# Performance work log

Hardware: AMD Instinct MI355X
Metric: run time of the kernel (lower is better)

The kernel has to match this reference:

```python
import jax, jax.numpy as jnp
import numpy as np

ROPE_THETA = 10000.0

def apply_rope(x, positions):
    # x: [b, h, s, d], positions: [s]
    d = x.shape[-1]
    inv_freq = ROPE_THETA ** (-jnp.arange(0, d, 2, dtype=jnp.float32) / d)  # [d/2]
    ang = positions.astype(jnp.float32)[:, None] * inv_freq[None, :]        # [s, d/2]
    cos = jnp.cos(ang)
    sin = jnp.sin(ang)
    x1 = x[..., 0::2]
    x2 = x[..., 1::2]
    r1 = x1 * cos - x2 * sin
    r2 = x1 * sin + x2 * cos
    # interleave back to [..., d]
    return jnp.stack([r1, r2], axis=-1).reshape(x.shape)

def setup_inputs() -> dict:
    key = jax.random.key(0)
    k1, k2, k3 = jax.random.split(key, 3)
    b, s, d_model = 4, 2048, 1024
    x = jax.random.normal(k1, (b, s, d_model), dtype=jnp.float32)
    wqkv = jax.random.normal(k2, (3 * d_model, d_model), dtype=jnp.float32) * (d_model ** -0.5)
    wo = jax.random.normal(k3, (d_model, d_model), dtype=jnp.float32) * (d_model ** -0.5)
    token_positions = jnp.arange(s, dtype=jnp.int64 if jax.config.jax_enable_x64 else jnp.int32)
    return {"x": x, "wqkv": wqkv, "wo": wo, "token_positions": token_positions}

def reference(x, wqkv, wo, token_positions):
    b, s, d_model = x.shape
    num_heads = 16
    d_head = d_model // num_heads
    # fused QKV projection (Linear: y = x @ W.T)
    qkv = jnp.einsum('bse,fe->bsf', x, wqkv)  # [b, s, 3*d_model]
    q, k, v = jnp.split(qkv, 3, axis=-1)
    def to_heads(t):
        return t.reshape(b, s, num_heads, d_head).transpose(0, 2, 1, 3)  # [b, h, s, d]
    q, k, v = to_heads(q), to_heads(k), to_heads(v)
    q = apply_rope(q, token_positions)
    k = apply_rope(k, token_positions)
    scores = jnp.einsum('bhqd,bhkd->bhqk', q, k) / jnp.sqrt(jnp.asarray(d_head, dtype=x.dtype))
    causal = jnp.tril(jnp.ones((s, s), dtype=bool))  # [s, s]
    scores = jnp.where(causal, scores, -jnp.inf)
    weights = jax.nn.softmax(scores, axis=-1)
    y = jnp.einsum('bhqk,bhkd->bhqd', weights, v)
    y = y.transpose(0, 2, 1, 3).reshape(b, s, d_model)
    return jnp.einsum('bse,fe->bsf', y, wo)
```

## Files before the change

### kernel.cpp

```cpp
#include <hip/hip_runtime.h>
#include <stdint.h>


typedef __attribute__((ext_vector_type(8))) short bf16x8;
typedef __attribute__((ext_vector_type(4))) float f32x4;
typedef __attribute__((ext_vector_type(8))) unsigned short u16x8;
typedef __attribute__((ext_vector_type(4))) unsigned short u16x4;

#define NB 4
#define NS 2048
#define NH 16
#define DH 64
#define DM 1024
#define BH (NB*NH)

static __device__ __forceinline__ unsigned short f2bf(float f){
  unsigned u = __builtin_bit_cast(unsigned, f);
  u += 0x7fffu + ((u >> 16) & 1u);
  return (unsigned short)(u >> 16);
}
static __device__ __forceinline__ float bf2f(unsigned short h){
  unsigned u = ((unsigned)h) << 16;
  return __builtin_bit_cast(float, u);
}
static __device__ __forceinline__ unsigned cvt_pk_bf16(float lo, float hi){
  unsigned r;
  asm("v_cvt_pk_bf16_f32 %0, %1, %2" : "=v"(r) : "v"(lo), "v"(hi));
  return r;
}
static __device__ __forceinline__ f32x4 mfma16(bf16x8 a, bf16x8 b, f32x4 c){
  return __builtin_amdgcn_mfma_f32_16x16x32_bf16(a, b, c, 0, 0, 0);
}
static __device__ __forceinline__ void gld_lds16(const void* g, void* l){
  __builtin_amdgcn_global_load_lds((const __attribute__((address_space(1))) unsigned int*)g,
                                   (__attribute__((address_space(3))) unsigned int*)l,
                                   16, 0, 0);
}

__global__ __launch_bounds__(256) void cvt_all(const float* __restrict__ x,
                                               const float* __restrict__ wqkv,
                                               const float* __restrict__ wo,
                                               unsigned short* __restrict__ xb,
                                               unsigned short* __restrict__ wqkvb,
                                               unsigned short* __restrict__ wob){
  int stride = gridDim.x * blockDim.x;
  for (int i = blockIdx.x * blockDim.x + threadIdx.x; i < 3145728; i += stride){
    const float* src; unsigned short* dst; int j;
    if (i < 2097152){ src = x; dst = xb; j = i; }
    else if (i < 2883584){ src = wqkv; dst = wqkvb; j = i - 2097152; }
    else { src = wo; dst = wob; j = i - 2883584; }
    f32x4 v = *(const f32x4*)(src + (size_t)j * 4);
    u16x4 o;
    o[0] = f2bf(v[0]); o[1] = f2bf(v[1]); o[2] = f2bf(v[2]); o[3] = f2bf(v[3]);
    *(u16x4*)(dst + (size_t)j * 4) = o;
  }
}

__global__ void rope_table(const int* __restrict__ pos,
                           float* __restrict__ ct, float* __restrict__ st){
  int t = blockIdx.x * 256 + threadIdx.x;
  int s = t >> 5, i = t & 31;
  float p = (float)pos[s];
  float freq = exp2f(-(float)(2 * i) * (13.287712379549449f / 64.f));
  float a = p * freq;
  ct[t] = cosf(a);
  st[t] = sinf(a);
}

__global__ __launch_bounds__(256) void rope_qk(unsigned short* __restrict__ buf,
                                               const float* __restrict__ ct,
                                               const float* __restrict__ st){
  size_t t  = (size_t)blockIdx.x * 256 + threadIdx.x;
  size_t e0 = t * 8;
  int dh0 = (int)(e0 & 63);
  int s   = (int)((e0 >> 6) & (NS - 1));
  u16x8 v = *(const u16x8*)(buf + e0);
  f32x4 c  = *(const f32x4*)(ct + s * 32 + (dh0 >> 1));
  f32x4 sn = *(const f32x4*)(st + s * 32 + (dh0 >> 1));
  u16x8 o;
#pragma unroll
  for (int i = 0; i < 4; i++){
    float x1 = bf2f(v[2*i]), x2 = bf2f(v[2*i+1]);
    o[2*i]   = f2bf(x1 * c[i] - x2 * sn[i]);
    o[2*i+1] = f2bf(x1 * sn[i] + x2 * c[i]);
  }
  *(u16x8*)(buf + e0) = o;
}

template<int BM, int BN, int MF, int NFR, int EPI, int RING>
__global__ __launch_bounds__((BM/(MF*16))*(BN/(NFR*16))*64, 2)
void gemm_ring(const unsigned short* __restrict__ A,
               const unsigned short* __restrict__ Bm,
               void* __restrict__ out0, void* __restrict__ out1,
               void* __restrict__ out2, int M, int N, int K){
  constexpr int WM = BM / (MF * 16);
  constexpr int WN = BN / (NFR * 16);
  constexpr int T  = WM * WN * 64;
  constexpr int LA = BM * 4 / T;
  constexpr int LB = BN * 4 / T;
  constexpr int L  = LA + LB;
  __shared__ __attribute__((aligned(16))) unsigned short As[RING][BM * 32];
  __shared__ __attribute__((aligned(16))) unsigned short Bs[RING][BN * 32];
  int tid = threadIdx.x;
  int w = tid >> 6, l = tid & 63;
  int lr = l & 15, lk = l >> 4;
  int m0 = blockIdx.y * BM, n0 = blockIdx.x * BN;
  int wr = (w / WN) * (MF * 16), wc = (w % WN) * (NFR * 16);

  const int nt = K >> 5;

  auto stage = [&](int t, int buf){
    int k0 = t * 32;
#pragma unroll
    for (int i = 0; i < LA; i++){
      int f = i * T + tid;
      int row = f >> 2, c = f & 3;
      int gc = (c ^ ((row >> 1) & 3)) * 8;
      gld_lds16(A + (size_t)(m0 + row) * K + k0 + gc, &As[buf][(i * T + w * 64) * 8]);
    }
#pragma unroll
    for (int i = 0; i < LB; i++){
      int f = i * T + tid;
      int row = f >> 2, c = f & 3;
      int gc = (c ^ ((row >> 1) & 3)) * 8;
      gld_lds16(Bm + (size_t)(n0 + row) * K + k0 + gc, &Bs[buf][(i * T + w * 64) * 8]);
    }
  };

  f32x4 zero = {0.f, 0.f, 0.f, 0.f};
  f32x4 acc[MF][NFR];
#pragma unroll
  for (int a = 0; a < MF; a++)
#pragma unroll
    for (int b = 0; b < NFR; b++) acc[a][b] = zero;

#pragma unroll
  for (int p = 0; p < RING - 1; p++) stage(p, p);
  asm volatile("s_waitcnt vmcnt(%0)" :: "i"((RING - 2) * L) : "memory");
  __builtin_amdgcn_sched_barrier(0);
  __builtin_amdgcn_s_barrier();
  __builtin_amdgcn_sched_barrier(0);

  int buf = 0;
  for (int t = 0; t < nt; ++t){
    bf16x8 af[MF], bfr[NFR];
#pragma unroll
    for (int mf = 0; mf < MF; mf++){
      int row = wr + mf * 16 + lr;
      af[mf] = *(const bf16x8*)&As[buf][row * 32 + ((lk ^ ((row >> 1) & 3)) * 8)];
    }
#pragma unroll
    for (int nf = 0; nf < NFR; nf++){
      int row = wc + nf * 16 + lr;
      bfr[nf] = *(const bf16x8*)&Bs[buf][row * 32 + ((lk ^ ((row >> 1) & 3)) * 8)];
    }
    if (t + RING - 1 < nt){
      int sb = buf - 1; if (sb < 0) sb = RING - 1;
      stage(t + RING - 1, sb);
    }
    __builtin_amdgcn_s_setprio(1);
#pragma unroll
    for (int mf = 0; mf < MF; mf++)
#pragma unroll
      for (int nf = 0; nf < NFR; nf++)
        acc[mf][nf] = mfma16(af[mf], bfr[nf], acc[mf][nf]);
    __builtin_amdgcn_s_setprio(0);
    if (RING >= 4){
      if (t + 3 < nt)      { asm volatile("s_waitcnt vmcnt(%0)" :: "i"(2 * L) : "memory"); }
      else if (t + 2 < nt) { asm volatile("s_waitcnt vmcnt(%0)" :: "i"(L) : "memory"); }
      else if (t + 1 < nt) { asm volatile("s_waitcnt vmcnt(0)" ::: "memory"); }
    } else {
      if (t + 2 < nt)      { asm volatile("s_waitcnt vmcnt(%0)" :: "i"(L) : "memory"); }
      else if (t + 1 < nt) { asm volatile("s_waitcnt vmcnt(0)" ::: "memory"); }
    }
    __builtin_amdgcn_sched_barrier(0);
    __builtin_amdgcn_s_barrier();
    __builtin_amdgcn_sched_barrier(0);
    buf = buf + 1; if (buf == RING) buf = 0;
  }

  if (EPI == 0){
    unsigned short* q  = (unsigned short*)out0;
    unsigned short* k  = (unsigned short*)out1;
    unsigned short* vt = (unsigned short*)out2;
#pragma unroll
    for (int mf = 0; mf < MF; mf++)
#pragma unroll
      for (int nf = 0; nf < NFR; nf++)
#pragma unroll
        for (int j = 0; j < 4; j++){
          int m = m0 + wr + mf * 16 + lk * 4 + j;
          int n = n0 + wc + nf * 16 + lr;
          int part = n >> 10, c = n & 1023;
          int h = c >> 6, dh = c & 63;
          int b = m >> 11, s = m & (NS - 1);
          unsigned short val = f2bf(acc[mf][nf][j]);
          if (part == 2){
            vt[((size_t)((b * NH + h) * DH + dh)) * NS + s] = val;
          } else {
            size_t off = ((size_t)(b * NH + h) * NS + s) * DH + dh;
            ((part == 0) ? q : k)[off] = val;
          }
        }
  } else {
    float* C = (float*)out0;
#pragma unroll
    for (int mf = 0; mf < MF; mf++)
#pragma unroll
      for (int nf = 0; nf < NFR; nf++)
#pragma unroll
        for (int j = 0; j < 4; j++){
          int m = m0 + wr + mf * 16 + lk * 4 + j;
          int n = n0 + wc + nf * 16 + lr;
          C[(size_t)m * N + n] = acc[mf][nf][j];
        }
  }
}

__global__ __launch_bounds__(256, 3) void fa_kernel(const unsigned short* __restrict__ qb_,
                                                    const unsigned short* __restrict__ kbuf,
                                                    const unsigned short* __restrict__ vtb,
                                                    unsigned short* __restrict__ yb){
  __shared__ __attribute__((aligned(16))) unsigned short Kl[2][4096];
  __shared__ __attribute__((aligned(16))) unsigned short Vl[2][4096];
  __shared__ __attribute__((aligned(16))) unsigned short Pl[4][32 * 76];
  int tid = threadIdx.x;
  int w = tid >> 6, l = tid & 63;
  int lr = l & 15, lk = l >> 4;
  int qb = 15 - blockIdx.y;
  int bh = blockIdx.x;
  int b = bh >> 4, h = bh & 15;
  int qr0 = qb * 128 + w * 32;
  const unsigned short* Q  = qb_  + (size_t)bh * NS * DH;
  const unsigned short* Kp = kbuf + (size_t)bh * NS * DH;
  const unsigned short* VT = vtb  + (size_t)bh * DH * NS;
  unsigned short* Pw = &Pl[w][0];

  int r8  = l >> 3;
  int swc = ((l & 7) ^ (r8 & 7)) * 8;

  auto stage = [&](int buf, int t){
    int kbase = t * 64;
    if (w < 2){
#pragma unroll
      for (int ii = 0; ii < 4; ii++){
        int i = w * 4 + ii;
        gld_lds16(Kp + (size_t)(kbase + i * 8 + r8) * DH + swc, &Kl[buf][i * 512]);
      }
    } else {
#pragma unroll
      for (int ii = 0; ii < 4; ii++){
        int i = (w - 2) * 4 + ii;
        gld_lds16(VT + (size_t)(i * 8 + r8) * NS + kbase + swc, &Vl[buf][i * 512]);
      }
    }
  };

  bf16x8 qf[2][2];
#pragma unroll
  for (int mf = 0; mf < 2; mf++)
#pragma unroll
    for (int ks = 0; ks < 2; ks++)
      qf[mf][ks] = *(const bf16x8*)(Q + (size_t)(qr0 + mf * 16 + lr) * DH + ks * 32 + lk * 8);

  f32x4 zero = {0.f, 0.f, 0.f, 0.f};
  f32x4 O[2][4];
  float lsum[2];
#pragma unroll
  for (int mf = 0; mf < 2; mf++){
#pragma unroll
    for (int nf = 0; nf < 4; nf++) O[mf][nf] = zero;
    lsum[mf] = 0.f;
  }

  const float SC = 0.18033688011112042f;
  const int ntile = 2 * qb + 2;

  stage(0, 0);
  __syncthreads();

  int cur = 0;
  for (int t = 0; t < ntile; ++t){
    int kbase = t * 64;
    if (t + 1 < ntile) stage(cur ^ 1, t + 1);

    if (kbase <= qr0 + 31){
      bf16x8 kf[4][2];
#pragma unroll
      for (int nf = 0; nf < 4; nf++){
        int row = nf * 16 + lr;
        int ro = row * 64, sw = (row & 7) << 3;
#pragma unroll
        for (int ks = 0; ks < 2; ks++)
          kf[nf][ks] = *(const bf16x8*)&Kl[cur][ro + ((ks * 32 + lk * 8) ^ sw)];
      }
      bf16x8 vf[2][4];
#pragma unroll
      for (int nfd = 0; nfd < 4; nfd++){
        int row = nfd * 16 + lr;
        int ro = row * 64, sw = (row & 7) << 3;
#pragma unroll
        for (int ks = 0; ks < 2; ks++)
          vf[ks][nfd] = *(const bf16x8*)&Vl[cur][ro + ((ks * 32 + lk * 8) ^ sw)];
      }

      f32x4 sa[2][4];
#pragma unroll
      for (int mf = 0; mf < 2; mf++)
#pragma unroll
        for (int nf = 0; nf < 4; nf++) sa[mf][nf] = zero;
#pragma unroll
      for (int nf = 0; nf < 4; nf++)
#pragma unroll
        for (int mf = 0; mf < 2; mf++){
          sa[mf][nf] = mfma16(kf[nf][0], qf[mf][0], sa[mf][nf]);
          sa[mf][nf] = mfma16(kf[nf][1], qf[mf][1], sa[mf][nf]);
        }

      bool domask = (kbase + 63 > qr0);

#pragma unroll
      for (int mf = 0; mf < 2; mf++){
        int qg = qr0 + mf * 16 + lr;
        float ls = 0.f;
#pragma unroll
        for (int nf = 0; nf < 4; nf++){
          float p4[4];
#pragma unroll
          for (int j = 0; j < 4; j++){
            float xx = __builtin_fmaf(sa[mf][nf][j], SC, -8.0f);
            if (domask){
              int kg = kbase + nf * 16 + lk * 4 + j;
              if (kg > qg) xx = -__builtin_inff();
            }
            float p = exp2f(xx);
            ls += p;
            p4[j] = p;
          }
          unsigned d0 = cvt_pk_bf16(p4[0], p4[1]);
          unsigned d1 = cvt_pk_bf16(p4[2], p4[3]);
          int base = (mf * 16 + lr) * 76 + nf * 16 + lk * 4;
          *(unsigned*)&Pw[base]     = d0;
          *(unsigned*)&Pw[base + 2] = d1;
        }
        lsum[mf] += ls;
      }

      bf16x8 pf[2][2];
#pragma unroll
      for (int mf = 0; mf < 2; mf++)
#pragma unroll
        for (int ks = 0; ks < 2; ks++)
          pf[mf][ks] = *(const bf16x8*)&Pw[(mf * 16 + lr) * 76 + ks * 32 + lk * 8];
#pragma unroll
      for (int ks = 0; ks < 2; ks++)
#pragma unroll
        for (int nfd = 0; nfd < 4; nfd++)
#pragma unroll
          for (int mf = 0; mf < 2; mf++)
            O[mf][nfd] = mfma16(pf[mf][ks], vf[ks][nfd], O[mf][nfd]);
    }

    __syncthreads();
    cur ^= 1;
  }

#pragma unroll
  for (int mf = 0; mf < 2; mf++){
    lsum[mf] += __shfl_xor(lsum[mf], 16);
    lsum[mf] += __shfl_xor(lsum[mf], 32);
  }
#pragma unroll
  for (int mf = 0; mf < 2; mf++)
#pragma unroll
    for (int j = 0; j < 4; j++){
      float s = __shfl(lsum[mf], lk * 4 + j);
      float inv = 1.0f / s;
      int srow = qr0 + mf * 16 + lk * 4 + j;
      unsigned short* yp = yb + ((size_t)(b * NS + srow)) * DM + h * DH;
#pragma unroll
      for (int nfd = 0; nfd < 4; nfd++)
        yp[nfd * 16 + lr] = f2bf(O[mf][nfd][j] * inv);
    }
}

extern "C" void kernel_launch(void* const* d_in, const int* in_sizes, int n_in,
                              void* d_out, int out_size, void* d_ws, size_t ws_size,
                              hipStream_t stream){
  const float* x    = (const float*)d_in[0];
  const float* wqkv = (const float*)d_in[1];
  const float* wo   = (const float*)d_in[2];
  const int*   pos  = (const int*)d_in[3];
  float* out = (float*)d_out;

  char* ws = (char*)d_ws;
  size_t off = 0;
  auto alloc = [&](size_t bytes) -> void* {
    void* p = ws + off;
    off += (bytes + 255) & ~(size_t)255;
    return p;
  };
  const size_t NE = (size_t)BH * NS * DH;
  unsigned short* xb    = (unsigned short*)alloc((size_t)8192 * 1024 * 2);
  unsigned short* wqkvb = (unsigned short*)alloc((size_t)3072 * 1024 * 2);
  unsigned short* wob   = (unsigned short*)alloc((size_t)1024 * 1024 * 2);
  unsigned short* q  = (unsigned short*)alloc(NE * 2);
  unsigned short* k  = (unsigned short*)alloc(NE * 2);
  unsigned short* vt = (unsigned short*)alloc(NE * 2);
  unsigned short* y  = (unsigned short*)alloc(NE * 2);
  float* ct = (float*)alloc((size_t)NS * 32 * 4);
  float* st = (float*)alloc((size_t)NS * 32 * 4);

  cvt_all<<<3072, 256, 0, stream>>>(x, wqkv, wo, xb, wqkvb, wob);
  rope_table<<<256, 256, 0, stream>>>(pos, ct, st);
  gemm_ring<128, 256, 8, 4, 0, 3><<<dim3(12, 64), 256, 0, stream>>>(
      xb, wqkvb, q, k, vt, 8192, 3072, 1024);
  rope_qk<<<4096, 256, 0, stream>>>(q, ct, st);
  rope_qk<<<4096, 256, 0, stream>>>(k, ct, st);
  fa_kernel<<<dim3(64, 16), 256, 0, stream>>>(q, k, vt, y);
  gemm_ring<128, 128, 4, 4, 1, 4><<<dim3(8, 64), 256, 0, stream>>>(
      y, wob, out, nullptr, nullptr, 8192, 1024, 1024);
}
```

Before: 228.4 us.

## Load V fragments directly from global in attention and retune GEMM tiles

The attention kernel no longer stages V^T tiles through LDS. Each wave reads its V fragments straight from global memory, and all four waves now share the K staging. This cuts LDS use, shrinks the P scratch padding, and raises the occupancy hint to 4. The QKV GEMM moves from 128x256 to 128x128 tiles with more blocks and an occupancy hint of 3. The trade-off is that V loads now come from global or L2 inside the inner loop with their latency exposed, and the P padding change may cause LDS bank conflicts.

```diff
diff --git a/kernel.cpp b/kernel.cpp
--- a/kernel.cpp
+++ b/kernel.cpp
@@ -87,8 +87,8 @@
   *(u16x8*)(buf + e0) = o;
 }
 
-template<int BM, int BN, int MF, int NFR, int EPI, int RING>
-__global__ __launch_bounds__((BM/(MF*16))*(BN/(NFR*16))*64, 2)
+template<int BM, int BN, int MF, int NFR, int EPI, int RING, int OCC>
+__global__ __launch_bounds__((BM/(MF*16))*(BN/(NFR*16))*64, OCC)
 void gemm_ring(const unsigned short* __restrict__ A,
                const unsigned short* __restrict__ Bm,
                void* __restrict__ out0, void* __restrict__ out1,
@@ -217,13 +217,12 @@
   }
 }
 
-__global__ __launch_bounds__(256, 3) void fa_kernel(const unsigned short* __restrict__ qb_,
+__global__ __launch_bounds__(256, 4) void fa_kernel(const unsigned short* __restrict__ qb_,
                                                     const unsigned short* __restrict__ kbuf,
                                                     const unsigned short* __restrict__ vtb,
                                                     unsigned short* __restrict__ yb){
   __shared__ __attribute__((aligned(16))) unsigned short Kl[2][4096];
-  __shared__ __attribute__((aligned(16))) unsigned short Vl[2][4096];
-  __shared__ __attribute__((aligned(16))) unsigned short Pl[4][32 * 76];
+  __shared__ __attribute__((aligned(16))) unsigned short Pl[4][32 * 72];
   int tid = threadIdx.x;
   int w = tid >> 6, l = tid & 63;
   int lr = l & 15, lk = l >> 4;
@@ -241,18 +240,10 @@
 
   auto stage = [&](int buf, int t){
     int kbase = t * 64;
-    if (w < 2){
-#pragma unroll
-      for (int ii = 0; ii < 4; ii++){
-        int i = w * 4 + ii;
-        gld_lds16(Kp + (size_t)(kbase + i * 8 + r8) * DH + swc, &Kl[buf][i * 512]);
-      }
-    } else {
-#pragma unroll
-      for (int ii = 0; ii < 4; ii++){
-        int i = (w - 2) * 4 + ii;
-        gld_lds16(VT + (size_t)(i * 8 + r8) * NS + kbase + swc, &Vl[buf][i * 512]);
-      }
+#pragma unroll
+    for (int ii = 0; ii < 2; ii++){
+      int i = w * 2 + ii;
+      gld_lds16(Kp + (size_t)(kbase + i * 8 + r8) * DH + swc, &Kl[buf][i * 512]);
     }
   };
 
@@ -285,6 +276,13 @@
     if (t + 1 < ntile) stage(cur ^ 1, t + 1);
 
     if (kbase <= qr0 + 31){
+      bf16x8 vf[2][4];
+#pragma unroll
+      for (int ks = 0; ks < 2; ks++)
+#pragma unroll
+        for (int nfd = 0; nfd < 4; nfd++)
+          vf[ks][nfd] = *(const bf16x8*)(VT + (size_t)(nfd * 16 + lr) * NS + kbase + ks * 32 + lk * 8);
+
       bf16x8 kf[4][2];
 #pragma unroll
       for (int nf = 0; nf < 4; nf++){
@@ -293,15 +291,6 @@
 #pragma unroll
         for (int ks = 0; ks < 2; ks++)
           kf[nf][ks] = *(const bf16x8*)&Kl[cur][ro + ((ks * 32 + lk * 8) ^ sw)];
-      }
-      bf16x8 vf[2][4];
-#pragma unroll
-      for (int nfd = 0; nfd < 4; nfd++){
-        int row = nfd * 16 + lr;
-        int ro = row * 64, sw = (row & 7) << 3;
-#pragma unroll
-        for (int ks = 0; ks < 2; ks++)
-          vf[ks][nfd] = *(const bf16x8*)&Vl[cur][ro + ((ks * 32 + lk * 8) ^ sw)];
       }
 
       f32x4 sa[2][4];
@@ -337,11 +326,10 @@
             ls += p;
             p4[j] = p;
           }
-          unsigned d0 = cvt_pk_bf16(p4[0], p4[1]);
-          unsigned d1 = cvt_pk_bf16(p4[2], p4[3]);
-          int base = (mf * 16 + lr) * 76 + nf * 16 + lk * 4;
-          *(unsigned*)&Pw[base]     = d0;
-          *(unsigned*)&Pw[base + 2] = d1;
+          uint2 dd;
+          dd.x = cvt_pk_bf16(p4[0], p4[1]);
+          dd.y = cvt_pk_bf16(p4[2], p4[3]);
+          *(uint2*)&Pw[(mf * 16 + lr) * 72 + nf * 16 + lk * 4] = dd;
         }
         lsum[mf] += ls;
       }
@@ -351,7 +339,7 @@
       for (int mf = 0; mf < 2; mf++)
 #pragma unroll
         for (int ks = 0; ks < 2; ks++)
-          pf[mf][ks] = *(const bf16x8*)&Pw[(mf * 16 + lr) * 76 + ks * 32 + lk * 8];
+          pf[mf][ks] = *(const bf16x8*)&Pw[(mf * 16 + lr) * 72 + ks * 32 + lk * 8];
 #pragma unroll
       for (int ks = 0; ks < 2; ks++)
 #pragma unroll
@@ -413,11 +401,11 @@
 
   cvt_all<<<3072, 256, 0, stream>>>(x, wqkv, wo, xb, wqkvb, wob);
   rope_table<<<256, 256, 0, stream>>>(pos, ct, st);
-  gemm_ring<128, 256, 8, 4, 0, 3><<<dim3(12, 64), 256, 0, stream>>>(
+  gemm_ring<128, 128, 4, 4, 0, 3, 3><<<dim3(24, 64), 256, 0, stream>>>(
       xb, wqkvb, q, k, vt, 8192, 3072, 1024);
   rope_qk<<<4096, 256, 0, stream>>>(q, ct, st);
   rope_qk<<<4096, 256, 0, stream>>>(k, ct, st);
   fa_kernel<<<dim3(64, 16), 256, 0, stream>>>(q, k, vt, y);
-  gemm_ring<128, 128, 4, 4, 1, 4><<<dim3(8, 64), 256, 0, stream>>>(
+  gemm_ring<128, 128, 4, 4, 1, 4, 2><<<dim3(8, 64), 256, 0, stream>>>(
       y, wob, out, nullptr, nullptr, 8192, 1024, 1024);
 }
```

After: 252.7 us. +10.7%, slower.

## Fuse Q RoPE into attention Q load and retile QKV GEMM

Applied to the files above, without the earlier changes.

Removes the separate RoPE pass over Q by applying the rotation with the cos/sin tables while loading Q fragments inside the attention kernel, which saves a full read-modify-write of the Q buffer. It also changes the QKV projection GEMM from 128x256 to 128x128 tiles with a doubled grid and an occupancy hint of 3, via a new OCC template parameter on launch bounds. The extra rotation math in the attention prologue is small. The smaller GEMM tiles give more blocks and occupancy but less data reuse per tile.

```diff
diff --git a/kernel.cpp b/kernel.cpp
--- a/kernel.cpp
+++ b/kernel.cpp
@@ -6,6 +6,7 @@
 typedef __attribute__((ext_vector_type(4))) float f32x4;
 typedef __attribute__((ext_vector_type(8))) unsigned short u16x8;
 typedef __attribute__((ext_vector_type(4))) unsigned short u16x4;
+typedef __attribute__((ext_vector_type(4))) unsigned int u32x4;
 
 #define NB 4
 #define NS 2048
@@ -87,8 +88,8 @@
   *(u16x8*)(buf + e0) = o;
 }
 
-template<int BM, int BN, int MF, int NFR, int EPI, int RING>
-__global__ __launch_bounds__((BM/(MF*16))*(BN/(NFR*16))*64, 2)
+template<int BM, int BN, int MF, int NFR, int EPI, int RING, int OCC>
+__global__ __launch_bounds__((BM/(MF*16))*(BN/(NFR*16))*64, OCC)
 void gemm_ring(const unsigned short* __restrict__ A,
                const unsigned short* __restrict__ Bm,
                void* __restrict__ out0, void* __restrict__ out1,
@@ -220,7 +221,9 @@
 __global__ __launch_bounds__(256, 3) void fa_kernel(const unsigned short* __restrict__ qb_,
                                                     const unsigned short* __restrict__ kbuf,
                                                     const unsigned short* __restrict__ vtb,
-                                                    unsigned short* __restrict__ yb){
+                                                    unsigned short* __restrict__ yb,
+                                                    const float* __restrict__ ct_,
+                                                    const float* __restrict__ st_){
   __shared__ __attribute__((aligned(16))) unsigned short Kl[2][4096];
   __shared__ __attribute__((aligned(16))) unsigned short Vl[2][4096];
   __shared__ __attribute__((aligned(16))) unsigned short Pl[4][32 * 76];
@@ -258,10 +261,25 @@
 
   bf16x8 qf[2][2];
 #pragma unroll
-  for (int mf = 0; mf < 2; mf++)
-#pragma unroll
-    for (int ks = 0; ks < 2; ks++)
-      qf[mf][ks] = *(const bf16x8*)(Q + (size_t)(qr0 + mf * 16 + lr) * DH + ks * 32 + lk * 8);
+  for (int mf = 0; mf < 2; mf++){
+    int srow = qr0 + mf * 16 + lr;
+    const unsigned short* qrow = Q + (size_t)srow * DH;
+    const float* ctr = ct_ + srow * 32;
+    const float* str = st_ + srow * 32;
+#pragma unroll
+    for (int ks = 0; ks < 2; ks++){
+      u16x8 raw = *(const u16x8*)(qrow + ks * 32 + lk * 8);
+      f32x4 cc = *(const f32x4*)(ctr + ks * 16 + lk * 4);
+      f32x4 ss = *(const f32x4*)(str + ks * 16 + lk * 4);
+      u32x4 wds;
+#pragma unroll
+      for (int p = 0; p < 4; p++){
+        float x1 = bf2f(raw[2*p]), x2 = bf2f(raw[2*p+1]);
+        wds[p] = cvt_pk_bf16(x1 * cc[p] - x2 * ss[p], x1 * ss[p] + x2 * cc[p]);
+      }
+      qf[mf][ks] = __builtin_bit_cast(bf16x8, wds);
+    }
+  }
 
   f32x4 zero = {0.f, 0.f, 0.f, 0.f};
   f32x4 O[2][4];
@@ -413,11 +431,10 @@
 
   cvt_all<<<3072, 256, 0, stream>>>(x, wqkv, wo, xb, wqkvb, wob);
   rope_table<<<256, 256, 0, stream>>>(pos, ct, st);
-  gemm_ring<128, 256, 8, 4, 0, 3><<<dim3(12, 64), 256, 0, stream>>>(
+  gemm_ring<128, 128, 4, 4, 0, 3, 3><<<dim3(24, 64), 256, 0, stream>>>(
       xb, wqkvb, q, k, vt, 8192, 3072, 1024);
-  rope_qk<<<4096, 256, 0, stream>>>(q, ct, st);
   rope_qk<<<4096, 256, 0, stream>>>(k, ct, st);
-  fa_kernel<<<dim3(64, 16), 256, 0, stream>>>(q, k, vt, y);
-  gemm_ring<128, 128, 4, 4, 1, 4><<<dim3(8, 64), 256, 0, stream>>>(
+  fa_kernel<<<dim3(64, 16), 256, 0, stream>>>(q, k, vt, y, ct, st);
+  gemm_ring<128, 128, 4, 4, 1, 4, 2><<<dim3(8, 64), 256, 0, stream>>>(
       y, wob, out, nullptr, nullptr, 8192, 1024, 1024);
 }
```

Result: faster. 218.3 us (-4.4%).
